# Optimization experiments

Measured on AMD Instinct MI355X. Metric: run time of the kernel, lower is better.

The kernel has to match this reference:

```python
import jax, jax.numpy as jnp
import numpy as np

N_SUPPORT = 65536
N_QUERY = 65536
FEAT = 1024
EMBED = 512
WAYS = 256


def setup_inputs() -> dict:
    key = jax.random.key(0)
    k1, k2, k3, k4 = jax.random.split(key, 4)
    support_images = jax.random.normal(k1, (N_SUPPORT, FEAT), dtype=jnp.float32)
    query_images = jax.random.normal(k2, (N_QUERY, FEAT), dtype=jnp.float32)
    # deterministic labels so every one of the `ways` classes is non-empty
    labels = jnp.arange(N_SUPPORT, dtype=jnp.int32) % WAYS
    support_labels = jax.nn.one_hot(labels, WAYS, dtype=jnp.int32)  # one-hot, as in torch forward
    W = jax.random.normal(k3, (FEAT, EMBED), dtype=jnp.float32) / np.sqrt(FEAT).astype(np.float32)
    b = jax.random.normal(k4, (EMBED,), dtype=jnp.float32) * 0.01
    return {
        "support_images": support_images,
        "support_labels": support_labels,
        "query_images": query_images,
        "W": W,
        "b": b,
    }


def reference(support_images, support_labels, query_images, W, b):
    ways = support_labels.shape[1]
    labels = jnp.argmax(support_labels, axis=1)  # [N_support]

    # backbone: Linear(feat -> embed)
    z_support = support_images @ W + b  # [N_support, E]
    z_query = query_images @ W + b      # [N_query, E]

    # fused per-class mean (replaces the python loop over classes)
    sums = jax.ops.segment_sum(z_support, labels, num_segments=ways)          # [ways, E]
    counts = jax.ops.segment_sum(jnp.ones((z_support.shape[0],), z_support.dtype),
                                 labels, num_segments=ways)                   # [ways]
    z_proto = sums / counts[:, None]

    # scores = -cdist(z_query, z_proto)  (euclidean, p=2)
    q2 = jnp.sum(z_query * z_query, axis=1, keepdims=True)   # [Nq, 1]
    p2 = jnp.sum(z_proto * z_proto, axis=1)[None, :]          # [1, ways]
    d2 = q2 + p2 - 2.0 * (z_query @ z_proto.T)                # [Nq, ways]
    scores = -jnp.sqrt(jnp.maximum(d2, 0.0))

    return jax.nn.softmax(scores, axis=1)
```

## Files before the change

### kernel.cpp

```cpp
#include <hip/hip_runtime.h>
#include <stdint.h>

#define NSUP 65536
#define NQRY 65536
#define FEAT 1024
#define EMB  512
#define WAYS 256

typedef unsigned short u16;
typedef unsigned int   u32;
typedef __attribute__((ext_vector_type(8))) __bf16 bf16x8;
typedef __attribute__((ext_vector_type(4))) float  f32x4;

static __device__ __forceinline__ u16 f2bf(float f) {
    u32 u = __builtin_bit_cast(u32, f);
    u32 r = u + 0x7fffu + ((u >> 16) & 1u);
    return (u16)(r >> 16);
}

static __device__ __forceinline__ void gl_lds16(const void* g, void* l) {
    __builtin_amdgcn_global_load_lds((const __attribute__((address_space(1))) u32*)g,
                                     (__attribute__((address_space(3))) u32*)l,
                                     16, 0, 0);
}

static __device__ __forceinline__ int swz16(int r, int s) {
    return r * 32 + ((s ^ ((r >> 1) & 3)) * 8);
}

__global__ __launch_bounds__(256) void k0_transpose(const float* __restrict__ W,
                                                    u16* __restrict__ Wt,
                                                    int* __restrict__ icounts) {
    const int t = threadIdx.x;
    if (blockIdx.x == 0) icounts[t] = 0;
    __shared__ float tile[64][65];
    const int bx = blockIdx.x;
    const int k0 = (bx & 15) * 64;
    const int e0 = (bx >> 4) * 64;
#pragma unroll
    for (int i = 0; i < 16; ++i) {
        int idx = t + i * 256;
        int kk = idx >> 6, ee = idx & 63;
        tile[kk][ee] = W[(size_t)(k0 + kk) * EMB + e0 + ee];
    }
    __syncthreads();
#pragma unroll
    for (int i = 0; i < 16; ++i) {
        int idx = t + i * 256;
        int ee = idx >> 6, kk = idx & 63;
        Wt[(size_t)(e0 + ee) * FEAT + k0 + kk] = f2bf(tile[kk][ee]);
    }
}

__global__ __launch_bounds__(256) void k1a_labels(const int* __restrict__ sl,
                                                  int* __restrict__ labels,
                                                  int* __restrict__ icounts) {
    const int row = blockIdx.x * 4 + (threadIdx.x >> 6);
    const int lane = threadIdx.x & 63;
    const int4* p = (const int4*)(sl + (size_t)row * WAYS);
    int4 v = p[lane];
    int my = -1;
    if (v.x) my = lane * 4 + 0;
    if (v.y) my = lane * 4 + 1;
    if (v.z) my = lane * 4 + 2;
    if (v.w) my = lane * 4 + 3;
#pragma unroll
    for (int m = 32; m; m >>= 1) my = max(my, __shfl_xor(my, m));
    if (lane == 0) {
        labels[row] = my;
        atomicAdd(&icounts[my], 1);
    }
}

__global__ __launch_bounds__(256) void k1p_prefix(const int* __restrict__ icounts,
                                                  int* __restrict__ offs,
                                                  int* __restrict__ cursor,
                                                  float* __restrict__ countsF) {
    __shared__ int s[256];
    const int t = threadIdx.x;
    const int v = icounts[t];
    s[t] = v;
    __syncthreads();
    for (int d = 1; d < 256; d <<= 1) {
        int x = (t >= d) ? s[t - d] : 0;
        __syncthreads();
        s[t] += x;
        __syncthreads();
    }
    const int exc = s[t] - v;
    offs[t] = exc;
    cursor[t] = exc;
    countsF[t] = (float)v;
}

__global__ __launch_bounds__(256) void k1s_scatter(const int* __restrict__ labels,
                                                   int* __restrict__ cursor,
                                                   int* __restrict__ perm) {
    const int r = blockIdx.x * 256 + threadIdx.x;
    const int lb = labels[r];
    const int pos = atomicAdd(&cursor[lb], 1);
    perm[pos] = r;
}

__global__ __launch_bounds__(256) void k1c_classsum(const float* __restrict__ img,
                                                    const int* __restrict__ perm,
                                                    const int* __restrict__ offs,
                                                    const int* __restrict__ icounts,
                                                    float* __restrict__ sums) {
    const int c  = blockIdx.x >> 2;
    const int fs = blockIdx.x & 3;
    const int t  = threadIdx.x;
    const int base = offs[c];
    const int n    = icounts[c];
    const size_t fcol = (size_t)fs * 256 + t;
    float acc = 0.f;
    int i = 0;
    for (; i + 8 <= n; i += 8) {
        int rr[8];
#pragma unroll
        for (int u = 0; u < 8; ++u) rr[u] = perm[base + i + u];
        float v[8];
#pragma unroll
        for (int u = 0; u < 8; ++u) v[u] = img[(size_t)rr[u] * FEAT + fcol];
#pragma unroll
        for (int u = 0; u < 8; ++u) acc += v[u];
    }
    for (; i < n; ++i) acc += img[(size_t)perm[base + i] * FEAT + fcol];
    sums[(size_t)c * FEAT + fcol] = acc;
}

__global__ __launch_bounds__(512) void k2_proto(const float* __restrict__ sums,
                                                const float* __restrict__ counts,
                                                const float* __restrict__ W,
                                                u16* __restrict__ zpb,
                                                float* __restrict__ p2) {
    __shared__ float proto[FEAT];
    __shared__ float red[8];
    const int c = blockIdx.x, t = threadIdx.x;
    const float inv = 1.0f / counts[c];
    proto[t]       = sums[(size_t)c * FEAT + t] * inv;
    proto[t + 512] = sums[(size_t)c * FEAT + t + 512] * inv;
    __syncthreads();
    float a0 = 0.f, a1 = 0.f, a2 = 0.f, a3 = 0.f;
#pragma unroll 8
    for (int k = 0; k < FEAT; k += 4) {
        a0 += proto[k + 0] * W[(size_t)(k + 0) * EMB + t];
        a1 += proto[k + 1] * W[(size_t)(k + 1) * EMB + t];
        a2 += proto[k + 2] * W[(size_t)(k + 2) * EMB + t];
        a3 += proto[k + 3] * W[(size_t)(k + 3) * EMB + t];
    }
    float z = (a0 + a1) + (a2 + a3);
    zpb[(size_t)c * EMB + t] = f2bf(z);
    float sq = z * z;
#pragma unroll
    for (int m = 1; m < 64; m <<= 1) sq += __shfl_xor(sq, m);
    if ((t & 63) == 0) red[t >> 6] = sq;
    __syncthreads();
    if (t == 0) {
        float s = 0.f;
#pragma unroll
        for (int i = 0; i < 8; ++i) s += red[i];
        p2[c] = s;
    }
}

__global__ __launch_bounds__(1024, 4) void k3_zq(const float* __restrict__ Q,
                                                 const u16* __restrict__ Wt,
                                                 u16* __restrict__ zq,
                                                 float* __restrict__ q2p) {
    __shared__ u16 Asl[2][128 * 32];
    __shared__ u16 Bsl[2][512 * 32];
    const int t = threadIdx.x;
    const int lane = t & 63, wave = t >> 6;
    const int wm = wave >> 3, wn = wave & 7;
    const int L = lane & 15, g = lane >> 4;
    const size_t row0 = (size_t)blockIdx.x * 128;

    const int ar = t >> 2, as = t & 3;
    const float* aptr = Q + (row0 + ar) * FEAT + as * 8;
    const int aw = swz16(ar, as);
    float af[8];

    auto loadA = [&](int ks) {
        const float4* p = (const float4*)(aptr + ks * 32);
        float4 x = p[0], y = p[1];
        af[0] = x.x; af[1] = x.y; af[2] = x.z; af[3] = x.w;
        af[4] = y.x; af[5] = y.y; af[6] = y.z; af[7] = y.w;
    };
    auto writeA = [&](int buf) {
        uint4 w;
        w.x = (u32)f2bf(af[0]) | ((u32)f2bf(af[1]) << 16);
        w.y = (u32)f2bf(af[2]) | ((u32)f2bf(af[3]) << 16);
        w.z = (u32)f2bf(af[4]) | ((u32)f2bf(af[5]) << 16);
        w.w = (u32)f2bf(af[6]) | ((u32)f2bf(af[7]) << 16);
        *(uint4*)&Asl[buf][aw] = w;
    };
    auto stageB = [&](int buf, int ks) {
#pragma unroll
        for (int p = 0; p < 2; ++p) {
            int gi = t + p * 1024;
            int r = gi >> 2, cc = gi & 3;
            int s = cc ^ ((r >> 1) & 3);
            gl_lds16(Wt + (size_t)r * FEAT + ks * 32 + s * 8, &Bsl[buf][gi * 8]);
        }
    };

    f32x4 acc[4][4];
#pragma unroll
    for (int mt = 0; mt < 4; ++mt)
#pragma unroll
        for (int nt = 0; nt < 4; ++nt) acc[mt][nt] = f32x4{0.f, 0.f, 0.f, 0.f};

    stageB(0, 0);
    if (t < 512) { loadA(0); writeA(0); }
    __syncthreads();

    const int ard = swz16(wm * 64 + L, g);
    const int brd = swz16(wn * 64 + L, g);

    int cur = 0;
    for (int ks = 0; ks < 32; ++ks) {
        const int nxt = cur ^ 1;
        if (ks < 31) {
            stageB(nxt, ks + 1);
            if (t < 512) loadA(ks + 1);
        }
        bf16x8 a[4], b[4];
#pragma unroll
        for (int mt = 0; mt < 4; ++mt) a[mt] = *(const bf16x8*)&Asl[cur][ard + mt * 512];
#pragma unroll
        for (int nt = 0; nt < 4; ++nt) b[nt] = *(const bf16x8*)&Bsl[cur][brd + nt * 512];
#pragma unroll
        for (int mt = 0; mt < 4; ++mt)
#pragma unroll
            for (int nt = 0; nt < 4; ++nt)
                acc[mt][nt] = __builtin_amdgcn_mfma_f32_16x16x32_bf16(a[mt], b[nt], acc[mt][nt], 0, 0, 0);
        if (ks < 31 && t < 512) writeA(nxt);
        __syncthreads();
        cur = nxt;
    }

    const int c = L;
#pragma unroll
    for (int mt = 0; mt < 4; ++mt) {
#pragma unroll
        for (int j = 0; j < 4; ++j) {
            const int rloc = wm * 64 + mt * 16 + g * 4 + j;
            const size_t r = row0 + rloc;
            float ss = 0.f;
#pragma unroll
            for (int nt = 0; nt < 4; ++nt) {
                float v = acc[mt][nt][j];
                ss += v * v;
                zq[r * EMB + wn * 64 + nt * 16 + c] = f2bf(v);
            }
#pragma unroll
            for (int m = 1; m < 16; m <<= 1) ss += __shfl_xor(ss, m);
            if (c == 0) q2p[(size_t)wn * NQRY + r] = ss;
        }
    }
}

__global__ __launch_bounds__(512, 4) void k4_scores(const u16* __restrict__ zq,
                                                    const u16* __restrict__ zp,
                                                    const float* __restrict__ q2p,
                                                    const float* __restrict__ p2,
                                                    float* __restrict__ out) {
    __shared__ u16 Asl[2][128 * 32];
    __shared__ u16 Bsl[2][256 * 32];
    __shared__ float p2l[WAYS];
    __shared__ float q2s[128];
    const int t = threadIdx.x;
    const int lane = t & 63, wave = t >> 6;
    const int wm = wave >> 2, wn = wave & 3;
    const size_t row0 = (size_t)blockIdx.x * 128;
    if (t < WAYS) p2l[t] = p2[t];
    if (t >= WAYS && t < WAYS + 128) {
        int r = t - WAYS;
        float s0 = 0.f;
#pragma unroll
        for (int p = 0; p < 8; ++p) s0 += q2p[(size_t)p * NQRY + row0 + r];
        q2s[r] = s0;
    }

    auto stage = [&](int buf, int ks) {
        { int r = t >> 2, cc = t & 3;
          int s = cc ^ ((r >> 1) & 3);
          gl_lds16(zq + (row0 + r) * EMB + ks * 32 + s * 8, &Asl[buf][t * 8]); }
#pragma unroll
        for (int p = 0; p < 2; ++p) {
            int gi = t + p * 512;
            int r = gi >> 2, cc = gi & 3;
            int s = cc ^ ((r >> 1) & 3);
            gl_lds16(zp + (size_t)r * EMB + ks * 32 + s * 8, &Bsl[buf][gi * 8]);
        }
    };

    f32x4 acc[4][4];
#pragma unroll
    for (int mt = 0; mt < 4; ++mt)
#pragma unroll
        for (int nt = 0; nt < 4; ++nt) acc[mt][nt] = f32x4{0.f, 0.f, 0.f, 0.f};

    stage(0, 0);
    __syncthreads();

    const int L = lane & 15, g = lane >> 4;
    const int ard = swz16(wm * 64 + L, g);
    const int brd = swz16(wn * 64 + L, g);

    int cur = 0;
    for (int ks = 0; ks < 16; ++ks) {
        const int nxt = cur ^ 1;
        if (ks < 15) stage(nxt, ks + 1);
        bf16x8 a[4], b[4];
#pragma unroll
        for (int mt = 0; mt < 4; ++mt) a[mt] = *(const bf16x8*)&Asl[cur][ard + mt * 512];
#pragma unroll
        for (int nt = 0; nt < 4; ++nt) b[nt] = *(const bf16x8*)&Bsl[cur][brd + nt * 512];
#pragma unroll
        for (int mt = 0; mt < 4; ++mt)
#pragma unroll
            for (int nt = 0; nt < 4; ++nt)
                acc[mt][nt] = __builtin_amdgcn_mfma_f32_16x16x32_bf16(a[mt], b[nt], acc[mt][nt], 0, 0, 0);
        __syncthreads();
        cur = nxt;
    }

    float* rmax = (float*)&Asl[0][0];
    float* rsum = rmax + 512;
    const int c = L;

#pragma unroll
    for (int mt = 0; mt < 4; ++mt)
#pragma unroll
        for (int j = 0; j < 4; ++j) {
            const int rloc = wm * 64 + mt * 16 + g * 4 + j;
            const float qv = q2s[rloc];
            float m_ = -1e30f;
#pragma unroll
            for (int nt = 0; nt < 4; ++nt) {
                float d2 = qv + p2l[wn * 64 + nt * 16 + c] - 2.f * acc[mt][nt][j];
                float s = -sqrtf(fmaxf(d2, 0.f));
                acc[mt][nt][j] = s;
                m_ = fmaxf(m_, s);
            }
#pragma unroll
            for (int m = 1; m < 16; m <<= 1) m_ = fmaxf(m_, __shfl_xor(m_, m));
            if (c == 0) rmax[rloc * 4 + wn] = m_;
        }
    __syncthreads();
#pragma unroll
    for (int mt = 0; mt < 4; ++mt)
#pragma unroll
        for (int j = 0; j < 4; ++j) {
            const int rloc = wm * 64 + mt * 16 + g * 4 + j;
            float m4 = fmaxf(fmaxf(rmax[rloc * 4 + 0], rmax[rloc * 4 + 1]),
                             fmaxf(rmax[rloc * 4 + 2], rmax[rloc * 4 + 3]));
            float s_ = 0.f;
#pragma unroll
            for (int nt = 0; nt < 4; ++nt) {
                float e = __expf(acc[mt][nt][j] - m4);
                acc[mt][nt][j] = e;
                s_ += e;
            }
#pragma unroll
            for (int m = 1; m < 16; m <<= 1) s_ += __shfl_xor(s_, m);
            if (c == 0) rsum[rloc * 4 + wn] = s_;
        }
    __syncthreads();
#pragma unroll
    for (int mt = 0; mt < 4; ++mt)
#pragma unroll
        for (int j = 0; j < 4; ++j) {
            const int rloc = wm * 64 + mt * 16 + g * 4 + j;
            float inv = 1.f / ((rsum[rloc * 4 + 0] + rsum[rloc * 4 + 1]) +
                               (rsum[rloc * 4 + 2] + rsum[rloc * 4 + 3]));
#pragma unroll
            for (int nt = 0; nt < 4; ++nt)
                out[(row0 + rloc) * WAYS + wn * 64 + nt * 16 + c] = acc[mt][nt][j] * inv;
        }
}

extern "C" void kernel_launch(void* const* d_in, const int* in_sizes, int n_in,
                              void* d_out, int out_size, void* d_ws, size_t ws_size,
                              hipStream_t stream) {
    (void)in_sizes; (void)n_in; (void)out_size; (void)ws_size;
    const float* simg = (const float*)d_in[0];
    const int*   slab = (const int*)d_in[1];
    const float* qimg = (const float*)d_in[2];
    const float* W    = (const float*)d_in[3];
    float* out = (float*)d_out;
    char* ws = (char*)d_ws;

    int*   labels = (int*)  (ws + 0);
    int*   perm   = (int*)  (ws + 262144);
    int*   icounts= (int*)  (ws + 524288);
    int*   offs   = (int*)  (ws + 525312);
    int*   cursor = (int*)  (ws + 526336);
    float* countsF= (float*)(ws + 527360);
    float* sums   = (float*)(ws + 528384);
    float* p2     = (float*)(ws + 1576960);
    u16*   zpb    = (u16*)  (ws + 1577984);
    u16*   Wt     = (u16*)  (ws + 1840128);
    u16*   zq     = (u16*)  (ws + 2888704);
    float* q2p    = (float*)(ws + 69997568);


    k0_transpose <<<128,        256, 0, stream>>>(W, Wt, icounts);
    k1a_labels   <<<NSUP / 4,   256, 0, stream>>>(slab, labels, icounts);
    k1p_prefix   <<<1,          256, 0, stream>>>(icounts, offs, cursor, countsF);
    k1s_scatter  <<<NSUP / 256, 256, 0, stream>>>(labels, cursor, perm);
    k1c_classsum <<<WAYS * 4,   256, 0, stream>>>(simg, perm, offs, icounts, sums);
    k2_proto     <<<WAYS,       512, 0, stream>>>(sums, countsF, W, zpb, p2);
    k3_zq        <<<NQRY / 128, 1024, 0, stream>>>(qimg, Wt, zq, q2p);
    k4_scores    <<<NQRY / 128, 512, 0, stream>>>(zq, zpb, q2p, p2, out);
}
```

Measured before the change: 363.8 us.

## Restructure score kernel to per-wave full-row tiles without LDS staging

The score kernel now gives each wave 16 query rows across all 256 classes. Operands are read directly from global memory instead of being staged through double-buffered LDS, so row max and sum need only in-wave shuffles and no block-level syncs. The q2 partial sums are reduced inside the projection kernel through shared memory, so only the final per-row value is written out. The cost is that each wave reloads the whole prototype matrix from global memory or cache with no LDS reuse, and each thread holds 64 accumulator registers.

```diff
diff --git a/kernel.cpp b/kernel.cpp
--- a/kernel.cpp
+++ b/kernel.cpp
@@ -167,7 +167,7 @@
 __global__ __launch_bounds__(1024, 4) void k3_zq(const float* __restrict__ Q,
                                                  const u16* __restrict__ Wt,
                                                  u16* __restrict__ zq,
-                                                 float* __restrict__ q2p) {
+                                                 float* __restrict__ q2) {
     __shared__ u16 Asl[2][128 * 32];
     __shared__ u16 Bsl[2][512 * 32];
     const int t = threadIdx.x;
@@ -240,6 +240,7 @@
         cur = nxt;
     }
 
+    float* q2part = (float*)&Asl[0][0];
     const int c = L;
 #pragma unroll
     for (int mt = 0; mt < 4; ++mt) {
@@ -256,130 +257,85 @@
             }
 #pragma unroll
             for (int m = 1; m < 16; m <<= 1) ss += __shfl_xor(ss, m);
-            if (c == 0) q2p[(size_t)wn * NQRY + r] = ss;
-        }
-    }
-}
-
-__global__ __launch_bounds__(512, 4) void k4_scores(const u16* __restrict__ zq,
+            if (c == 0) q2part[wn * 128 + rloc] = ss;
+        }
+    }
+    __syncthreads();
+    if (t < 128) {
+        float s0 = 0.f;
+#pragma unroll
+        for (int p = 0; p < 8; ++p) s0 += q2part[p * 128 + t];
+        q2[row0 + t] = s0;
+    }
+}
+
+__global__ __launch_bounds__(256, 4) void k4_scores(const u16* __restrict__ zq,
                                                     const u16* __restrict__ zp,
-                                                    const float* __restrict__ q2p,
+                                                    const float* __restrict__ q2,
                                                     const float* __restrict__ p2,
                                                     float* __restrict__ out) {
-    __shared__ u16 Asl[2][128 * 32];
-    __shared__ u16 Bsl[2][256 * 32];
-    __shared__ float p2l[WAYS];
-    __shared__ float q2s[128];
     const int t = threadIdx.x;
     const int lane = t & 63, wave = t >> 6;
-    const int wm = wave >> 2, wn = wave & 3;
-    const size_t row0 = (size_t)blockIdx.x * 128;
-    if (t < WAYS) p2l[t] = p2[t];
-    if (t >= WAYS && t < WAYS + 128) {
-        int r = t - WAYS;
-        float s0 = 0.f;
-#pragma unroll
-        for (int p = 0; p < 8; ++p) s0 += q2p[(size_t)p * NQRY + row0 + r];
-        q2s[r] = s0;
-    }
-
-    auto stage = [&](int buf, int ks) {
-        { int r = t >> 2, cc = t & 3;
-          int s = cc ^ ((r >> 1) & 3);
-          gl_lds16(zq + (row0 + r) * EMB + ks * 32 + s * 8, &Asl[buf][t * 8]); }
-#pragma unroll
-        for (int p = 0; p < 2; ++p) {
-            int gi = t + p * 512;
-            int r = gi >> 2, cc = gi & 3;
-            int s = cc ^ ((r >> 1) & 3);
-            gl_lds16(zp + (size_t)r * EMB + ks * 32 + s * 8, &Bsl[buf][gi * 8]);
-        }
-    };
-
-    f32x4 acc[4][4];
-#pragma unroll
-    for (int mt = 0; mt < 4; ++mt)
-#pragma unroll
-        for (int nt = 0; nt < 4; ++nt) acc[mt][nt] = f32x4{0.f, 0.f, 0.f, 0.f};
-
-    stage(0, 0);
-    __syncthreads();
-
     const int L = lane & 15, g = lane >> 4;
-    const int ard = swz16(wm * 64 + L, g);
-    const int brd = swz16(wn * 64 + L, g);
-
-    int cur = 0;
+    const size_t row0 = (size_t)blockIdx.x * 64 + wave * 16;
+
+    float p2v[16];
+#pragma unroll
+    for (int nt = 0; nt < 16; ++nt) p2v[nt] = p2[nt * 16 + L];
+    float q2v[4];
+#pragma unroll
+    for (int j = 0; j < 4; ++j) q2v[j] = q2[row0 + g * 4 + j];
+
+    f32x4 acc[16];
+#pragma unroll
+    for (int nt = 0; nt < 16; ++nt) acc[nt] = f32x4{0.f, 0.f, 0.f, 0.f};
+
+    const u16* arow = zq + (row0 + L) * EMB;
+
     for (int ks = 0; ks < 16; ++ks) {
-        const int nxt = cur ^ 1;
-        if (ks < 15) stage(nxt, ks + 1);
-        bf16x8 a[4], b[4];
-#pragma unroll
-        for (int mt = 0; mt < 4; ++mt) a[mt] = *(const bf16x8*)&Asl[cur][ard + mt * 512];
-#pragma unroll
-        for (int nt = 0; nt < 4; ++nt) b[nt] = *(const bf16x8*)&Bsl[cur][brd + nt * 512];
-#pragma unroll
-        for (int mt = 0; mt < 4; ++mt)
-#pragma unroll
-            for (int nt = 0; nt < 4; ++nt)
-                acc[mt][nt] = __builtin_amdgcn_mfma_f32_16x16x32_bf16(a[mt], b[nt], acc[mt][nt], 0, 0, 0);
-        __syncthreads();
-        cur = nxt;
-    }
-
-    float* rmax = (float*)&Asl[0][0];
-    float* rsum = rmax + 512;
-    const int c = L;
-
-#pragma unroll
-    for (int mt = 0; mt < 4; ++mt)
+        bf16x8 a = *(const bf16x8*)(arow + ks * 32 + g * 8);
+#pragma unroll
+        for (int nt = 0; nt < 16; ++nt) {
+            bf16x8 b = *(const bf16x8*)(zp + (size_t)(nt * 16 + L) * EMB + ks * 32 + g * 8);
+            acc[nt] = __builtin_amdgcn_mfma_f32_16x16x32_bf16(a, b, acc[nt], 0, 0, 0);
+        }
+    }
+
+    float mx[4] = {-1e30f, -1e30f, -1e30f, -1e30f};
+#pragma unroll
+    for (int nt = 0; nt < 16; ++nt)
 #pragma unroll
         for (int j = 0; j < 4; ++j) {
-            const int rloc = wm * 64 + mt * 16 + g * 4 + j;
-            const float qv = q2s[rloc];
-            float m_ = -1e30f;
-#pragma unroll
-            for (int nt = 0; nt < 4; ++nt) {
-                float d2 = qv + p2l[wn * 64 + nt * 16 + c] - 2.f * acc[mt][nt][j];
-                float s = -sqrtf(fmaxf(d2, 0.f));
-                acc[mt][nt][j] = s;
-                m_ = fmaxf(m_, s);
-            }
-#pragma unroll
-            for (int m = 1; m < 16; m <<= 1) m_ = fmaxf(m_, __shfl_xor(m_, m));
-            if (c == 0) rmax[rloc * 4 + wn] = m_;
-        }
-    __syncthreads();
-#pragma unroll
-    for (int mt = 0; mt < 4; ++mt)
+            float d2 = q2v[j] + p2v[nt] - 2.f * acc[nt][j];
+            float s = -sqrtf(fmaxf(d2, 0.f));
+            acc[nt][j] = s;
+            mx[j] = fmaxf(mx[j], s);
+        }
+#pragma unroll
+    for (int j = 0; j < 4; ++j)
+#pragma unroll
+        for (int m = 1; m < 16; m <<= 1) mx[j] = fmaxf(mx[j], __shfl_xor(mx[j], m));
+
+    float sm[4] = {0.f, 0.f, 0.f, 0.f};
+#pragma unroll
+    for (int nt = 0; nt < 16; ++nt)
 #pragma unroll
         for (int j = 0; j < 4; ++j) {
-            const int rloc = wm * 64 + mt * 16 + g * 4 + j;
-            float m4 = fmaxf(fmaxf(rmax[rloc * 4 + 0], rmax[rloc * 4 + 1]),
-                             fmaxf(rmax[rloc * 4 + 2], rmax[rloc * 4 + 3]));
-            float s_ = 0.f;
-#pragma unroll
-            for (int nt = 0; nt < 4; ++nt) {
-                float e = __expf(acc[mt][nt][j] - m4);
-                acc[mt][nt][j] = e;
-                s_ += e;
-            }
-#pragma unroll
-            for (int m = 1; m < 16; m <<= 1) s_ += __shfl_xor(s_, m);
-            if (c == 0) rsum[rloc * 4 + wn] = s_;
-        }
-    __syncthreads();
-#pragma unroll
-    for (int mt = 0; mt < 4; ++mt)
-#pragma unroll
-        for (int j = 0; j < 4; ++j) {
-            const int rloc = wm * 64 + mt * 16 + g * 4 + j;
-            float inv = 1.f / ((rsum[rloc * 4 + 0] + rsum[rloc * 4 + 1]) +
-                               (rsum[rloc * 4 + 2] + rsum[rloc * 4 + 3]));
-#pragma unroll
-            for (int nt = 0; nt < 4; ++nt)
-                out[(row0 + rloc) * WAYS + wn * 64 + nt * 16 + c] = acc[mt][nt][j] * inv;
-        }
+            float e = __expf(acc[nt][j] - mx[j]);
+            acc[nt][j] = e;
+            sm[j] += e;
+        }
+#pragma unroll
+    for (int j = 0; j < 4; ++j) {
+#pragma unroll
+        for (int m = 1; m < 16; m <<= 1) sm[j] += __shfl_xor(sm[j], m);
+        sm[j] = 1.f / sm[j];
+    }
+#pragma unroll
+    for (int nt = 0; nt < 16; ++nt)
+#pragma unroll
+        for (int j = 0; j < 4; ++j)
+            out[(row0 + g * 4 + j) * WAYS + nt * 16 + L] = acc[nt][j] * sm[j];
 }
 
 extern "C" void kernel_launch(void* const* d_in, const int* in_sizes, int n_in,
@@ -404,7 +360,7 @@
     u16*   zpb    = (u16*)  (ws + 1577984);
     u16*   Wt     = (u16*)  (ws + 1840128);
     u16*   zq     = (u16*)  (ws + 2888704);
-    float* q2p    = (float*)(ws + 69997568);
+    float* q2     = (float*)(ws + 69997568);
 
 
     k0_transpose <<<128,        256, 0, stream>>>(W, Wt, icounts);
@@ -413,6 +369,6 @@
     k1s_scatter  <<<NSUP / 256, 256, 0, stream>>>(labels, cursor, perm);
     k1c_classsum <<<WAYS * 4,   256, 0, stream>>>(simg, perm, offs, icounts, sums);
     k2_proto     <<<WAYS,       512, 0, stream>>>(sums, countsF, W, zpb, p2);
-    k3_zq        <<<NQRY / 128, 1024, 0, stream>>>(qimg, Wt, zq, q2p);
-    k4_scores    <<<NQRY / 128, 512, 0, stream>>>(zq, zpb, q2p, p2, out);
-}
+    k3_zq        <<<NQRY / 128, 1024, 0, stream>>>(qimg, Wt, zq, q2);
+    k4_scores    <<<NQRY / 64,  256, 0, stream>>>(zq, zpb, q2, p2, out);
+}
```

New measurement: 459.3 us. 26.3% more time.
